# Kernel optimization log

Measured on AMD Instinct MI355X. Metric: run time of the kernel, lower is better.

Reference implementation:

```python
import jax, jax.numpy as jnp
from jax import lax
import numpy as np

T, N, E = 8, 20000, 640000
D_IN, H, K = 2, 64, 3


def setup_inputs() -> dict:
    key = jax.random.key(0)
    ks = jax.random.split(key, 10)
    x = jax.random.normal(ks[0], (T, N, D_IN), dtype=jnp.float32)
    edge_idx = jax.random.randint(ks[1], (T, 2, E), 0, N, dtype=jnp.int64)
    edge_attr = jax.random.uniform(ks[2], (T, E), dtype=jnp.float32)
    Fin = D_IN + H
    s = 0.05
    Wr = jax.random.normal(ks[3], (K, Fin, H), dtype=jnp.float32) * s
    Wu = jax.random.normal(ks[4], (K, Fin, H), dtype=jnp.float32) * s
    Wc = jax.random.normal(ks[5], (K, Fin, H), dtype=jnp.float32) * s
    br = jnp.zeros((H,), dtype=jnp.float32)
    bu = jnp.zeros((H,), dtype=jnp.float32)
    bc = jnp.zeros((H,), dtype=jnp.float32)
    return {"x": x, "edge_idx": edge_idx, "edge_attr": edge_attr,
            "Wr": Wr, "br": br, "Wu": Wu, "bu": bu, "Wc": Wc, "bc": bc}


def reference(x, edge_idx, edge_attr, Wr, br, Wu, bu, Wc, bc):
    n = x.shape[1]
    k_hops = Wr.shape[0]

    def cheb(v, src, dst, wn, W, b):
        # Chebyshev recursion on scaled Laplacian (PyG ChebConv, lambda_max=2)
        def prop(t):
            return jax.ops.segment_sum(wn[:, None] * t[src], dst, num_segments=n)
        Tx0 = v
        out = Tx0 @ W[0]
        Tx1 = prop(Tx0)
        out = out + Tx1 @ W[1]
        for kk in range(2, k_hops):
            Tx2 = 2.0 * prop(Tx1) - Tx0
            out = out + Tx2 @ W[kk]
            Tx0, Tx1 = Tx1, Tx2
        return out + b

    def step(h, inp):
        x_t, ei, w_t = inp
        src, dst = ei[0], ei[1]
        # sym-normalized Laplacian, scaled by 2/lambda_max=1; self-loop weight is 0
        deg = jax.ops.segment_sum(w_t, src, num_segments=n)
        safe = jnp.where(deg > 0, deg, 1.0)
        dinv = jnp.where(deg > 0, lax.rsqrt(safe), 0.0)
        wn = -dinv[src] * w_t * dinv[dst]
        comb = jnp.concatenate([x_t, h], axis=1)
        r = jax.nn.sigmoid(cheb(comb, src, dst, wn, Wr, br))
        u = jax.nn.sigmoid(cheb(comb, src, dst, wn, Wu, bu))
        c = jnp.tanh(cheb(jnp.concatenate([x_t, r * h], axis=1), src, dst, wn, Wc, bc))
        h_new = u * h + (1.0 - u) * c
        return h_new, None

    h0 = jnp.zeros((n, br.shape[0]), dtype=x.dtype)
    h_final, _ = lax.scan(step, h0, (x, edge_idx, edge_attr))
    return h_final
```

## Files before the change

### kernel.cpp

```cpp
#include <hip/hip_runtime.h>

#define NN 20000
#define EE 640000
#define TT 8
#define HF 64
#define AS 232
#define ACS 104
#define BSS 194
#define PBLK 5000
#define TILE 2560
#define NBIN 250
#define BWID 80
#define ECAP 3072
#define LCAP 24

typedef _Float16 f16;
typedef unsigned int uint;
typedef __attribute__((ext_vector_type(8))) _Float16 half8;
typedef __attribute__((ext_vector_type(4))) float floatx4;

__device__ __forceinline__ float lo16f(uint v) { return (float)__builtin_bit_cast(f16, (unsigned short)(v & 0xffff)); }
__device__ __forceinline__ float hi16f(uint v) { return (float)__builtin_bit_cast(f16, (unsigned short)(v >> 16)); }
__device__ __forceinline__ uint pk16(float a, float b) {
    unsigned short ua = __builtin_bit_cast(unsigned short, (f16)a);
    unsigned short ub = __builtin_bit_cast(unsigned short, (f16)b);
    return (uint)ua | ((uint)ub << 16);
}

__global__ __launch_bounds__(256) void k_prepW(
    const float* __restrict__ Wr, const float* __restrict__ Wu, const float* __restrict__ Wc,
    f16* __restrict__ Wp, f16* __restrict__ Wcp)
{
    int idx = blockIdx.x * 256 + threadIdx.x;
    if (idx < 8 * 7 * 64) {
        int lane = idx & 63;
        int kb = (idx >> 6) % 7;
        int nb = (idx >> 6) / 7;
        int col = nb * 16 + (lane & 15);
        int g = col >> 6, jj = col & 63;
        const float* W = (g == 0) ? Wr : Wu;
        half8 v;
        #pragma unroll
        for (int e = 0; e < 8; e++) {
            int k = kb * 32 + ((lane >> 4) << 3) + e;
            float val = 0.f;
            if (k < 192)      { int hop = k >> 6; int i = 2 + (k & 63); val = W[(hop * 66 + i) * 64 + jj]; }
            else if (k < 198) { int q = k - 192;  int hop = q >> 1;     val = W[(hop * 66 + (q & 1)) * 64 + jj]; }
            v[e] = (f16)val;
        }
        *(half8*)&Wp[(size_t)idx * 8] = v;
        return;
    }
    int idx2 = idx - 8 * 7 * 64;
    if (idx2 >= 12 * 3 * 64) return;
    int lane = idx2 & 63;
    int kb = (idx2 >> 6) % 3;
    int nbc = (idx2 >> 6) / 3;
    int col = nbc * 16 + (lane & 15);
    int mode = col >> 6, j = col & 63;
    half8 v;
    #pragma unroll
    for (int e = 0; e < 8; e++) {
        int k = kb * 32 + ((lane >> 4) << 3) + e;
        float val = 0.f;
        if (k < 66) {
            if (mode == 0)      val = Wc[(0 * 66 + k) * 64 + j] - Wc[(2 * 66 + k) * 64 + j];
            else if (mode == 1) val = Wc[(1 * 66 + k) * 64 + j];
            else                val = Wc[(2 * 66 + k) * 64 + j];
        }
        v[e] = (f16)val;
    }
    *(half8*)&Wcp[(size_t)idx2 * 8] = v;
}

__global__ __launch_bounds__(256) void k_setx(
    const float* __restrict__ x4, uint* __restrict__ xf4,
    int* __restrict__ binptr, int* __restrict__ sbinptr)
{
    int idx = blockIdx.x * 256 + threadIdx.x;
    if (idx < 4 * NBIN) { binptr[idx] = 0; sbinptr[idx] = 0; }
    if (idx >= 4 * NN) return;
    int tl = idx / NN, n = idx - tl * NN;
    xf4[idx] = pk16(x4[(size_t)tl * NN * 2 + 2 * n], x4[(size_t)tl * NN * 2 + 2 * n + 1]);
}

__global__ __launch_bounds__(256) void k_bin(
    const int* __restrict__ eidx, const float* __restrict__ eatt, int t0,
    int* __restrict__ binptr, uint2* __restrict__ ebuf,
    int* __restrict__ sbinptr, uint* __restrict__ sbuf)
{
    __shared__ uint2 buf[NBIN][LCAP];
    __shared__ uint  sbl[NBIN][LCAP];
    __shared__ int lcnt[NBIN], scnt[NBIN];
    __shared__ int scan[256];
    __shared__ int gb[NBIN];
    int tid = threadIdx.x;
    if (tid < NBIN) { lcnt[tid] = 0; scnt[tid] = 0; }
    __syncthreads();
    int tl = blockIdx.x / 250, tile = blockIdx.x % 250;
    const int*   src = eidx + (size_t)(t0 + tl) * 2 * EE + tile * TILE;
    const int*   dst = src + EE;
    const float* w   = eatt + (size_t)(t0 + tl) * EE + tile * TILE;
    int* bp = binptr + tl * NBIN;
    int* sp = sbinptr + tl * NBIN;
    size_t ebase = (size_t)tl * NBIN * ECAP;
    #pragma unroll
    for (int i = 0; i < TILE / 256; i++) {
        int e = i * 256 + tid;
        int s = __builtin_nontemporal_load(&src[e]);
        int d = __builtin_nontemporal_load(&dst[e]);
        float wv = __builtin_nontemporal_load(&w[e]);
        int bin = d / BWID;
        uint2 ent = make_uint2(((uint)d << 16) | (uint)s, __float_as_uint(wv));
        int p = atomicAdd(&lcnt[bin], 1);
        if (p < LCAP) buf[bin][p] = ent;
        else {
            int gp = atomicAdd(&bp[bin], 1);
            if (gp < ECAP) ebuf[ebase + (size_t)bin * ECAP + gp] = ent;
        }
        int sbin = s / BWID;
        uint sent = (pk16(wv, 0.f) << 16) | (uint)s;
        int sq = atomicAdd(&scnt[sbin], 1);
        if (sq < LCAP) sbl[sbin][sq] = sent;
        else {
            int gp = atomicAdd(&sp[sbin], 1);
            if (gp < ECAP) sbuf[ebase + (size_t)sbin * ECAP + gp] = sent;
        }
    }
    __syncthreads();
    {
        int c = (tid < NBIN) ? (lcnt[tid] < LCAP ? lcnt[tid] : LCAP) : 0;
        scan[tid] = c;
        __syncthreads();
        #pragma unroll
        for (int o = 1; o < 256; o <<= 1) {
            int v = (tid >= o) ? scan[tid - o] : 0;
            __syncthreads();
            scan[tid] += v;
            __syncthreads();
        }
        if (c > 0) gb[tid] = atomicAdd(&bp[tid], c);
        __syncthreads();
        int total = scan[255];
        for (int i = tid; i < total; i += 256) {
            int lo = 0, hi = 255;
            #pragma unroll
            for (int it = 0; it < 8; it++) { int mid = (lo + hi) >> 1; if (scan[mid] > i) hi = mid; else lo = mid + 1; }
            int p = i - (lo ? scan[lo - 1] : 0);
            int gp = gb[lo] + p;
            if (gp < ECAP) ebuf[ebase + (size_t)lo * ECAP + gp] = buf[lo][p];
        }
    }
    __syncthreads();
    {
        int c = (tid < NBIN) ? (scnt[tid] < LCAP ? scnt[tid] : LCAP) : 0;
        scan[tid] = c;
        __syncthreads();
        #pragma unroll
        for (int o = 1; o < 256; o <<= 1) {
            int v = (tid >= o) ? scan[tid - o] : 0;
            __syncthreads();
            scan[tid] += v;
            __syncthreads();
        }
        if (c > 0) gb[tid] = atomicAdd(&sp[tid], c);
        __syncthreads();
        int total = scan[255];
        for (int i = tid; i < total; i += 256) {
            int lo = 0, hi = 255;
            #pragma unroll
            for (int it = 0; it < 8; it++) { int mid = (lo + hi) >> 1; if (scan[mid] > i) hi = mid; else lo = mid + 1; }
            int p = i - (lo ? scan[lo - 1] : 0);
            int gp = gb[lo] + p;
            if (gp < ECAP) sbuf[ebase + (size_t)lo * ECAP + gp] = sbl[lo][p];
        }
    }
}

__global__ __launch_bounds__(256) void k_degred(
    const uint* __restrict__ sbuf, const int* __restrict__ sbinptr,
    float* __restrict__ dinv)
{
    __shared__ float dacc[BWID];
    int tl = blockIdx.x / NBIN, b = blockIdx.x % NBIN, tid = threadIdx.x;
    int nume = sbinptr[tl * NBIN + b]; if (nume > ECAP) nume = ECAP;
    if (tid < BWID) dacc[tid] = 0.f;
    __syncthreads();
    size_t base = (size_t)(tl * NBIN + b) * ECAP;
    for (int i = tid; i < nume; i += 256) {
        uint e = sbuf[base + i];
        atomicAdd(&dacc[(e & 0xffff) - b * BWID], hi16f(e));
    }
    __syncthreads();
    if (tid < BWID) {
        float d = dacc[tid];
        dinv[(size_t)tl * NN + b * BWID + tid] = d > 0.f ? 1.f / sqrtf(d) : 0.f;
    }
}

__global__ __launch_bounds__(256) void k_csr(
    const uint2* __restrict__ ebuf, const int* __restrict__ binptr,
    const float* __restrict__ dinv,
    uint* __restrict__ entries, int* __restrict__ row_ptr, int* __restrict__ cnt)
{
    __shared__ uint proc[ECAP];
    __shared__ unsigned char lnb[ECAP];
    __shared__ uint staged[ECAP];
    __shared__ int lcnt[BWID], loff[BWID];
    int tl = blockIdx.x / NBIN, b = blockIdx.x % NBIN, tid = threadIdx.x;
    int nume = binptr[tl * NBIN + b]; if (nume > ECAP) nume = ECAP;
    const float* dv = dinv + (size_t)tl * NN;
    size_t base = (size_t)(tl * NBIN + b) * ECAP;
    if (tid < BWID) lcnt[tid] = 0;
    __syncthreads();
    for (int i = tid; i < nume; i += 256) {
        uint2 ent = ebuf[base + i];
        int s = ent.x & 0xffff;
        int d = ent.x >> 16;
        float wv = __uint_as_float(ent.y);
        float wn = -dv[s] * wv * dv[d];
        unsigned short wb = __builtin_bit_cast(unsigned short, (f16)wn);
        proc[i] = ((uint)wb << 16) | (uint)s;
        int ln = d - b * BWID;
        lnb[i] = (unsigned char)ln;
        atomicAdd(&lcnt[ln], 1);
    }
    __syncthreads();
    if (tid == 0) {
        int run = 0;
        for (int i = 0; i < BWID; i++) { loff[i] = run; run += lcnt[i]; }
    }
    __syncthreads();
    if (tid < BWID) {
        int n = tl * NN + b * BWID + tid;
        row_ptr[n] = (int)base + loff[tid];
        cnt[n] = lcnt[tid];
    }
    __syncthreads();
    for (int i = tid; i < nume; i += 256) {
        int p = atomicAdd(&loff[lnb[i]], 1);
        staged[p] = proc[i];
    }
    __syncthreads();
    for (int i = tid; i < nume; i += 256)
        entries[base + i] = staged[i];
}

__device__ __forceinline__ void gather64(
    const f16* __restrict__ src_mat, const uint* wnb, int mp, int j, int q,
    float& s0, float& s1)
{
    float a0[8], a1[8];
    #pragma unroll
    for (int k = 0; k < 8; k++) { a0[k] = 0.f; a1[k] = 0.f; }
    for (int e = 0; e < mp; e += 32) {
        uint ee[16], rr[16];
        #pragma unroll
        for (int k = 0; k < 16; k++) ee[k] = wnb[e + 2 * k + q];
        #pragma unroll
        for (int k = 0; k < 16; k++) rr[k] = *(const uint*)&src_mat[(size_t)(ee[k] & 0xffff) * HF + 2 * j];
        #pragma unroll
        for (int k = 0; k < 16; k++) {
            float w = hi16f(ee[k]);
            a0[k & 7] += w * lo16f(rr[k]);
            a1[k & 7] += w * hi16f(rr[k]);
        }
    }
    s0 = ((a0[0] + a0[1]) + (a0[2] + a0[3])) + ((a0[4] + a0[5]) + (a0[6] + a0[7]));
    s1 = ((a1[0] + a1[1]) + (a1[2] + a1[3])) + ((a1[4] + a1[5]) + (a1[6] + a1[7]));
    s0 += __shfl_xor(s0, 32);
    s1 += __shfl_xor(s1, 32);
}

__global__ __launch_bounds__(256) void k_prop(
    const f16* __restrict__ src_mat, const f16* __restrict__ base,
    f16* __restrict__ dst,
    const int* __restrict__ row_ptr, const int* __restrict__ cnt,
    const uint* __restrict__ entries,
    float alpha, float beta,
    const uint* __restrict__ xsrc, const uint* __restrict__ xbase,
    uint* __restrict__ xdst)
{
    __shared__ uint wnbuf[4][128];
    int ws = threadIdx.x >> 6, lane = threadIdx.x & 63;
    int node = blockIdx.x * 4 + ws;
    int m = cnt[node]; if (m > 128) m = 128;
    int st = row_ptr[node];
    int mp = (m + 31) & ~31;
    for (int idx = lane; idx < mp; idx += 64)
        wnbuf[ws][idx] = (idx < m) ? entries[st + idx] : 0u;
    asm volatile("s_waitcnt lgkmcnt(0)" ::: "memory");

    int j = lane & 31, q = lane >> 5;
    float s0, s1;
    gather64(src_mat, wnbuf[ws], mp, j, q, s0, s1);
    if (q == 0) {
        float r0 = alpha * s0, r1 = alpha * s1;
        if (base) {
            uint bv = *(const uint*)&base[(size_t)node * HF + 2 * j];
            r0 += beta * lo16f(bv);
            r1 += beta * hi16f(bv);
        }
        *(uint*)&dst[(size_t)node * HF + 2 * j] = pk16(r0, r1);
    }

    if (xdst) {
        float xa0 = 0.f, xa1 = 0.f;
        for (int i = lane; i < mp; i += 64) {
            uint ent = wnbuf[ws][i];
            uint xv = xsrc[ent & 0xffff];
            float wn = hi16f(ent);
            xa0 += wn * lo16f(xv);
            xa1 += wn * hi16f(xv);
        }
        #pragma unroll
        for (int o = 32; o >= 1; o >>= 1) {
            xa0 += __shfl_xor(xa0, o);
            xa1 += __shfl_xor(xa1, o);
        }
        if (lane == 0) {
            float r0 = alpha * xa0, r1 = alpha * xa1;
            if (xbase) { uint bv = xbase[node]; r0 += beta * lo16f(bv); r1 += beta * hi16f(bv); }
            xdst[node] = pk16(r0, r1);
        }
    }
}

__global__ __launch_bounds__(256) void k_prop_fin(
    const f16* __restrict__ S, const f16* __restrict__ B0,
    const f16* __restrict__ u, const float* __restrict__ h_in,
    float* __restrict__ h_out, f16* __restrict__ hA_out,
    const int* __restrict__ row_ptr, const int* __restrict__ cnt,
    const uint* __restrict__ entries)
{
    __shared__ uint wnbuf[4][128];
    int ws = threadIdx.x >> 6, lane = threadIdx.x & 63;
    int node = blockIdx.x * 4 + ws;
    int m = cnt[node]; if (m > 128) m = 128;
    int st = row_ptr[node];
    int mp = (m + 31) & ~31;
    for (int idx = lane; idx < mp; idx += 64)
        wnbuf[ws][idx] = (idx < m) ? entries[st + idx] : 0u;
    asm volatile("s_waitcnt lgkmcnt(0)" ::: "memory");

    int j = lane & 31, q = lane >> 5;
    float s0, s1;
    gather64(S, wnbuf[ws], mp, j, q, s0, s1);
    if (q == 0) {
        uint b0v = *(const uint*)&B0[(size_t)node * HF + 2 * j];
        float c0 = tanhf(s0 + lo16f(b0v));
        float c1 = tanhf(s1 + hi16f(b0v));
        uint uv = *(const uint*)&u[(size_t)node * HF + 2 * j];
        float u0 = lo16f(uv), u1 = hi16f(uv);
        float2 hv = *(const float2*)&h_in[(size_t)node * HF + 2 * j];
        float hn0 = u0 * hv.x + (1.f - u0) * c0;
        float hn1 = u1 * hv.y + (1.f - u1) * c1;
        *(float2*)&h_out[(size_t)node * HF + 2 * j] = make_float2(hn0, hn1);
        *(uint*)&hA_out[(size_t)node * HF + 2 * j] = pk16(hn0, hn1);
    }
}

#define MFMA16(a, b, c) __builtin_amdgcn_mfma_f32_16x16x32_f16(a, b, c, 0, 0, 0)

__global__ __launch_bounds__(512) void k_ru(
    const f16* __restrict__ hA, const f16* __restrict__ t1, const f16* __restrict__ t2,
    const uint* __restrict__ xf, const uint* __restrict__ t1x, const uint* __restrict__ t2x,
    const f16* __restrict__ Wp, const f16* __restrict__ Wcp,
    const float* __restrict__ br, const float* __restrict__ bu, const float* __restrict__ bc,
    f16* __restrict__ u_out,
    f16* __restrict__ B0, f16* __restrict__ B1, f16* __restrict__ B2)
{
    __shared__ __attribute__((aligned(16))) f16 At[64][AS];
    __shared__ __attribute__((aligned(16))) f16 Ac[64][ACS];
    __shared__ f16 Ub[64][68];
    int n0 = blockIdx.x * 64;
    int tid = threadIdx.x;

    for (int idx = tid; idx < 64 * 8 * 3; idx += 512) {
        int a = idx >> 9, r = (idx >> 3) & 63, s = idx & 7;
        const f16* src = (a == 0) ? hA : (a == 1 ? t1 : t2);
        int gn = n0 + r;
        half8 v = {0, 0, 0, 0, 0, 0, 0, 0};
        if (gn < NN) v = *(const half8*)&src[(size_t)gn * HF + s * 8];
        *(half8*)&At[r][a * 64 + s * 8] = v;
    }
    for (int idx = tid; idx < 64 * 17; idx += 512) {
        int r = idx / 17, c = idx % 17;
        *(uint*)((char*)&At[r][198] + 4 * c) = 0u;
    }
    for (int idx = tid; idx < 64 * 3; idx += 512) {
        int r = idx & 63, a = idx >> 6;
        const uint* src = (a == 0) ? xf : (a == 1 ? t1x : t2x);
        int gn = n0 + r;
        uint v = 0;
        if (gn < NN) v = src[gn];
        *(uint*)&At[r][192 + 2 * a] = v;
    }
    for (int idx = tid; idx < 64; idx += 512) {
        int gn = n0 + idx;
        *(uint*)&Ac[idx][0] = (gn < NN) ? xf[gn] : 0u;
    }
    for (int idx = tid; idx < 64 * 15; idx += 512) {
        int r = idx / 15, c = idx % 15;
        *(uint*)((char*)&Ac[r][66] + 4 * c) = 0u;
    }
    __syncthreads();

    int wid = tid >> 6, lane = tid & 63;
    int mrow = (wid & 1) * 32;
    int nb0 = (wid >> 1) * 2;
    int arow = mrow + (lane & 15);
    int koff = (lane >> 4) << 3;
    floatx4 z = {0.f, 0.f, 0.f, 0.f};
    {
        floatx4 acc00 = z, acc01 = z, acc10 = z, acc11 = z;
        #pragma unroll
        for (int kb = 0; kb < 7; kb++) {
            half8 a0 = *(const half8*)&At[arow][kb * 32 + koff];
            half8 a1 = *(const half8*)&At[arow + 16][kb * 32 + koff];
            half8 b0 = *(const half8*)&Wp[(size_t)(((nb0    ) * 7 + kb) * 64 + lane) * 8];
            half8 b1 = *(const half8*)&Wp[(size_t)(((nb0 + 1) * 7 + kb) * 64 + lane) * 8];
            acc00 = MFMA16(a0, b0, acc00);
            acc10 = MFMA16(a1, b0, acc10);
            acc01 = MFMA16(a0, b1, acc01);
            acc11 = MFMA16(a1, b1, acc11);
        }
        bool isR = nb0 < 4;
        #pragma unroll
        for (int mi = 0; mi < 2; mi++) {
            #pragma unroll
            for (int ni = 0; ni < 2; ni++) {
                floatx4 a = (mi == 0) ? (ni == 0 ? acc00 : acc01) : (ni == 0 ? acc10 : acc11);
                int jj = ((nb0 + ni) * 16 + (lane & 15)) & 63;
                float bias = isR ? br[jj] : bu[jj];
                int rbase = mrow + mi * 16 + ((lane >> 4) << 2);
                #pragma unroll
                for (int e = 0; e < 4; e++) {
                    int rloc = rbase + e;
                    float s = 1.f / (1.f + __expf(-(a[e] + bias)));
                    if (isR) {
                        float hv = (float)At[rloc][jj];
                        Ac[rloc][2 + jj] = (f16)(s * hv);
                    } else {
                        Ub[rloc][jj] = (f16)s;
                    }
                }
            }
        }
    }
    __syncthreads();

    for (int idx = tid; idx < 64 * 32; idx += 512) {
        int n = idx >> 5, c = idx & 31;
        int gn = n0 + n;
        if (gn < NN) *(uint*)&u_out[(size_t)gn * HF + 2 * c] = *(uint*)&Ub[n][2 * c];
    }
    f16* Bs = &At[0][0];
    #pragma unroll
    for (int i = 0; i < 6; i++) {
        int t = wid * 6 + i;
        int nbc = t >> 2, mq = t & 3;
        int ar = mq * 16 + (lane & 15);
        floatx4 acc;
        float binit = (nbc < 4) ? bc[nbc * 16 + (lane & 15)] : 0.f;
        acc[0] = binit; acc[1] = binit; acc[2] = binit; acc[3] = binit;
        #pragma unroll
        for (int kb = 0; kb < 3; kb++) {
            half8 a = *(const half8*)&Ac[ar][kb * 32 + koff];
            half8 b = *(const half8*)&Wcp[(size_t)(((nbc * 3 + kb) * 64) + lane) * 8];
            acc = MFMA16(a, b, acc);
        }
        int rbase = mq * 16 + ((lane >> 4) << 2);
        int col = nbc * 16 + (lane & 15);
        #pragma unroll
        for (int e = 0; e < 4; e++)
            Bs[(size_t)(rbase + e) * BSS + col] = (f16)acc[e];
    }
    __syncthreads();

    for (int idx = tid; idx < 64 * 96; idx += 512) {
        int n = idx / 96, c = idx % 96;
        int gn = n0 + n;
        if (gn < NN) {
            int col = 2 * c;
            f16* Bdst = (col < 64) ? B0 : (col < 128 ? B1 : B2);
            *(uint*)&Bdst[(size_t)gn * HF + (col & 63)] = *(uint*)&Bs[(size_t)n * BSS + col];
        }
    }
}


extern "C" void kernel_launch(void* const* d_in, const int* in_sizes, int n_in,
                              void* d_out, int out_size, void* d_ws, size_t ws_size,
                              hipStream_t stream)
{
    const float* x    = (const float*)d_in[0];
    const int*   eidx = (const int*)d_in[1];
    const float* eatt = (const float*)d_in[2];
    const float* Wr   = (const float*)d_in[3];
    const float* br   = (const float*)d_in[4];
    const float* Wu   = (const float*)d_in[5];
    const float* bu   = (const float*)d_in[6];
    const float* Wc   = (const float*)d_in[7];
    const float* bc   = (const float*)d_in[8];

    char* ws = (char*)d_ws;
    size_t off = 0;
    auto alloc = [&](size_t bytes) -> void* {
        void* p = ws + off;
        off += (bytes + 255) & ~(size_t)255;
        return p;
    };
    const size_t FB = (size_t)NN * HF * 2;
    float* h_f32   = (float*)alloc((size_t)NN * HF * 4);
    f16*   hA      = (f16*)alloc(FB);
    f16*   t1      = (f16*)alloc(FB);
    f16*   t2      = (f16*)alloc(FB);
    f16*   u       = (f16*)alloc(FB);
    f16*   B0      = (f16*)alloc(FB);
    f16*   B1      = (f16*)alloc(FB);
    f16*   B2      = (f16*)alloc(FB);
    float* dinv    = (float*)alloc((size_t)4 * NN * 4);
    uint*  xf      = (uint*)alloc((size_t)TT * NN * 4);
    uint*  t1x     = (uint*)alloc((size_t)NN * 4);
    uint*  t2x     = (uint*)alloc((size_t)NN * 4);
    int*   binptr  = (int*)alloc((size_t)4 * NBIN * 4);
    int*   sbinptr = (int*)alloc((size_t)4 * NBIN * 4);
    uint2* ebuf    = (uint2*)alloc((size_t)4 * NBIN * ECAP * 8);
    uint*  sbuf    = (uint*)alloc((size_t)4 * NBIN * ECAP * 4);
    uint*  entr    = (uint*)alloc((size_t)4 * NBIN * ECAP * 4);
    int*   rowp    = (int*)alloc((size_t)4 * NN * 4);
    int*   cnt     = (int*)alloc((size_t)4 * NN * 4);
    f16*   Wp      = (f16*)alloc((size_t)8 * 7 * 64 * 8 * 2);
    f16*   Wcp     = (f16*)alloc((size_t)12 * 3 * 64 * 8 * 2);

    hipMemsetAsync(h_f32, 0, (size_t)NN * HF * 4 + FB, stream);
    k_prepW<<<30, 256, 0, stream>>>(Wr, Wu, Wc, Wp, Wcp);

    const int GB = (NN + 63) / 64;
    const int DB = (4 * NN + 255) / 256;

    for (int half = 0; half < 2; ++half) {
        int t0 = half * 4;
        k_setx  <<<DB, 256, 0, stream>>>(x + (size_t)t0 * NN * 2, xf + (size_t)t0 * NN,
                                         binptr, sbinptr);
        k_bin   <<<1000, 256, 0, stream>>>(eidx, eatt, t0, binptr, ebuf, sbinptr, sbuf);
        k_degred<<<1000, 256, 0, stream>>>(sbuf, sbinptr, dinv);
        k_csr   <<<1000, 256, 0, stream>>>(ebuf, binptr, dinv, entr, rowp, cnt);

        for (int tl = 0; tl < 4; ++tl) {
            int t = t0 + tl;
            const int* rp = rowp + (size_t)tl * NN;
            const int* cp = cnt + (size_t)tl * NN;
            uint* xft = xf + (size_t)t * NN;

            k_prop<<<PBLK, 256, 0, stream>>>(hA, nullptr, t1, rp, cp, entr, 1.f,  0.f, xft, nullptr, t1x);
            k_prop<<<PBLK, 256, 0, stream>>>(t1, hA,      t2, rp, cp, entr, 2.f, -1.f, t1x, xft,     t2x);

            k_ru<<<GB, 512, 0, stream>>>(hA, t1, t2, xft, t1x, t2x, Wp, Wcp,
                                         br, bu, bc, u, B0, B1, B2);

            k_prop<<<PBLK, 256, 0, stream>>>(B2, B1, t2, rp, cp, entr, 2.f, 1.f, nullptr, nullptr, nullptr);

            float* hdst = (t == TT - 1) ? (float*)d_out : h_f32;
            k_prop_fin<<<PBLK, 256, 0, stream>>>(t2, B0, u, h_f32, hdst, hA, rp, cp, entr);
        }
    }
}
```

Measured before the change: 744.9 us.

## Replace global bin atomics with per-tile slot arrays and spill buffer

The edge binning kernel now writes each block's local per-bin buffers straight into fixed per-tile slots with per-tile counts, instead of scanning and using global atomics to compact into per-bin buffers. Overflow edges go to one small spill list per timestep, which the degree and CSR kernels scan and filter. The consumer kernels gather from 250 tile slots per bin and do a prefix scan to place entries. Timesteps are batched in groups of two instead of four, and x packing becomes a single upfront kernel. This trades contended global atomics and scan work in k_bin for more scattered reads in the consumers and a spill list that every block must scan.

```diff
diff --git a/kernel.cpp b/kernel.cpp
--- a/kernel.cpp
+++ b/kernel.cpp
@@ -13,9 +13,13 @@
 #define BWID 80
 #define ECAP 3072
 #define LCAP 24
+#define TB 2
+#define SPCAP 4096
 
 typedef _Float16 f16;
 typedef unsigned int uint;
+typedef unsigned char uchar;
+typedef unsigned long long ull;
 typedef __attribute__((ext_vector_type(8))) _Float16 half8;
 typedef __attribute__((ext_vector_type(4))) float floatx4;
 
@@ -73,27 +77,23 @@
     *(half8*)&Wcp[(size_t)idx2 * 8] = v;
 }
 
-__global__ __launch_bounds__(256) void k_setx(
-    const float* __restrict__ x4, uint* __restrict__ xf4,
-    int* __restrict__ binptr, int* __restrict__ sbinptr)
+__global__ __launch_bounds__(256) void k_pack(
+    const float* __restrict__ x, uint* __restrict__ xf)
 {
     int idx = blockIdx.x * 256 + threadIdx.x;
-    if (idx < 4 * NBIN) { binptr[idx] = 0; sbinptr[idx] = 0; }
-    if (idx >= 4 * NN) return;
-    int tl = idx / NN, n = idx - tl * NN;
-    xf4[idx] = pk16(x4[(size_t)tl * NN * 2 + 2 * n], x4[(size_t)tl * NN * 2 + 2 * n + 1]);
+    if (idx < TT * NN) xf[idx] = pk16(x[2 * idx], x[2 * idx + 1]);
 }
 
 __global__ __launch_bounds__(256) void k_bin(
     const int* __restrict__ eidx, const float* __restrict__ eatt, int t0,
-    int* __restrict__ binptr, uint2* __restrict__ ebuf,
-    int* __restrict__ sbinptr, uint* __restrict__ sbuf)
+    ull* __restrict__ dslot, uchar* __restrict__ dcnt_,
+    uint* __restrict__ sslot, uchar* __restrict__ scnt_,
+    ull* __restrict__ dsp, int* __restrict__ spn,
+    uint* __restrict__ ssp, int* __restrict__ ssn)
 {
     __shared__ uint2 buf[NBIN][LCAP];
     __shared__ uint  sbl[NBIN][LCAP];
     __shared__ int lcnt[NBIN], scnt[NBIN];
-    __shared__ int scan[256];
-    __shared__ int gb[NBIN];
     int tid = threadIdx.x;
     if (tid < NBIN) { lcnt[tid] = 0; scnt[tid] = 0; }
     __syncthreads();
@@ -101,9 +101,6 @@
     const int*   src = eidx + (size_t)(t0 + tl) * 2 * EE + tile * TILE;
     const int*   dst = src + EE;
     const float* w   = eatt + (size_t)(t0 + tl) * EE + tile * TILE;
-    int* bp = binptr + tl * NBIN;
-    int* sp = sbinptr + tl * NBIN;
-    size_t ebase = (size_t)tl * NBIN * ECAP;
     #pragma unroll
     for (int i = 0; i < TILE / 256; i++) {
         int e = i * 256 + tid;
@@ -111,85 +108,60 @@
         int d = __builtin_nontemporal_load(&dst[e]);
         float wv = __builtin_nontemporal_load(&w[e]);
         int bin = d / BWID;
-        uint2 ent = make_uint2(((uint)d << 16) | (uint)s, __float_as_uint(wv));
         int p = atomicAdd(&lcnt[bin], 1);
-        if (p < LCAP) buf[bin][p] = ent;
+        if (p < LCAP) buf[bin][p] = make_uint2(((uint)d << 16) | (uint)s, __float_as_uint(wv));
         else {
-            int gp = atomicAdd(&bp[bin], 1);
-            if (gp < ECAP) ebuf[ebase + (size_t)bin * ECAP + gp] = ent;
+            int gp = atomicAdd(&spn[tl], 1);
+            if (gp < SPCAP) dsp[(size_t)tl * SPCAP + gp] =
+                (ull)__float_as_uint(wv) << 32 | (((uint)d << 16) | (uint)s);
         }
         int sbin = s / BWID;
         uint sent = (pk16(wv, 0.f) << 16) | (uint)s;
         int sq = atomicAdd(&scnt[sbin], 1);
         if (sq < LCAP) sbl[sbin][sq] = sent;
         else {
-            int gp = atomicAdd(&sp[sbin], 1);
-            if (gp < ECAP) sbuf[ebase + (size_t)sbin * ECAP + gp] = sent;
-        }
-    }
-    __syncthreads();
-    {
-        int c = (tid < NBIN) ? (lcnt[tid] < LCAP ? lcnt[tid] : LCAP) : 0;
-        scan[tid] = c;
-        __syncthreads();
-        #pragma unroll
-        for (int o = 1; o < 256; o <<= 1) {
-            int v = (tid >= o) ? scan[tid - o] : 0;
-            __syncthreads();
-            scan[tid] += v;
-            __syncthreads();
-        }
-        if (c > 0) gb[tid] = atomicAdd(&bp[tid], c);
-        __syncthreads();
-        int total = scan[255];
-        for (int i = tid; i < total; i += 256) {
-            int lo = 0, hi = 255;
-            #pragma unroll
-            for (int it = 0; it < 8; it++) { int mid = (lo + hi) >> 1; if (scan[mid] > i) hi = mid; else lo = mid + 1; }
-            int p = i - (lo ? scan[lo - 1] : 0);
-            int gp = gb[lo] + p;
-            if (gp < ECAP) ebuf[ebase + (size_t)lo * ECAP + gp] = buf[lo][p];
-        }
-    }
-    __syncthreads();
-    {
-        int c = (tid < NBIN) ? (scnt[tid] < LCAP ? scnt[tid] : LCAP) : 0;
-        scan[tid] = c;
-        __syncthreads();
-        #pragma unroll
-        for (int o = 1; o < 256; o <<= 1) {
-            int v = (tid >= o) ? scan[tid - o] : 0;
-            __syncthreads();
-            scan[tid] += v;
-            __syncthreads();
-        }
-        if (c > 0) gb[tid] = atomicAdd(&sp[tid], c);
-        __syncthreads();
-        int total = scan[255];
-        for (int i = tid; i < total; i += 256) {
-            int lo = 0, hi = 255;
-            #pragma unroll
-            for (int it = 0; it < 8; it++) { int mid = (lo + hi) >> 1; if (scan[mid] > i) hi = mid; else lo = mid + 1; }
-            int p = i - (lo ? scan[lo - 1] : 0);
-            int gp = gb[lo] + p;
-            if (gp < ECAP) sbuf[ebase + (size_t)lo * ECAP + gp] = sbl[lo][p];
-        }
+            int gp = atomicAdd(&ssn[tl], 1);
+            if (gp < SPCAP) ssp[(size_t)tl * SPCAP + gp] = sent;
+        }
+    }
+    __syncthreads();
+    size_t base = (size_t)blockIdx.x * (NBIN * LCAP);
+    const ull* bufl = (const ull*)&buf[0][0];
+    for (int idx = tid; idx < NBIN * LCAP; idx += 256)
+        __builtin_nontemporal_store(bufl[idx], &dslot[base + idx]);
+    const uint* sbll = &sbl[0][0];
+    for (int idx = tid; idx < NBIN * LCAP; idx += 256)
+        __builtin_nontemporal_store(sbll[idx], &sslot[base + idx]);
+    if (tid < NBIN) {
+        dcnt_[blockIdx.x * 256 + tid] = (uchar)(lcnt[tid] < LCAP ? lcnt[tid] : LCAP);
+        scnt_[blockIdx.x * 256 + tid] = (uchar)(scnt[tid] < LCAP ? scnt[tid] : LCAP);
     }
 }
 
 __global__ __launch_bounds__(256) void k_degred(
-    const uint* __restrict__ sbuf, const int* __restrict__ sbinptr,
+    const uint* __restrict__ sslot, const uchar* __restrict__ scnt_,
+    const uint* __restrict__ ssp, const int* __restrict__ ssn,
     float* __restrict__ dinv)
 {
     __shared__ float dacc[BWID];
+    __shared__ uchar cs[256];
     int tl = blockIdx.x / NBIN, b = blockIdx.x % NBIN, tid = threadIdx.x;
-    int nume = sbinptr[tl * NBIN + b]; if (nume > ECAP) nume = ECAP;
     if (tid < BWID) dacc[tid] = 0.f;
-    __syncthreads();
-    size_t base = (size_t)(tl * NBIN + b) * ECAP;
-    for (int i = tid; i < nume; i += 256) {
-        uint e = sbuf[base + i];
-        atomicAdd(&dacc[(e & 0xffff) - b * BWID], hi16f(e));
+    if (tid < 256) cs[tid] = (tid < 250) ? scnt_[(tl * 250 + tid) * 256 + b] : 0;
+    __syncthreads();
+    for (int idx = tid; idx < 250 * LCAP; idx += 256) {
+        int t = idx / LCAP, p = idx % LCAP;
+        if (p < (int)cs[t]) {
+            uint e = __builtin_nontemporal_load(
+                &sslot[((size_t)(tl * 250 + t) * NBIN + b) * LCAP + p]);
+            atomicAdd(&dacc[(e & 0xffff) - b * BWID], hi16f(e));
+        }
+    }
+    int nsp = ssn[tl]; if (nsp > SPCAP) nsp = SPCAP;
+    for (int i = tid; i < nsp; i += 256) {
+        uint e = ssp[(size_t)tl * SPCAP + i];
+        int s = e & 0xffff;
+        if (s / BWID == b) atomicAdd(&dacc[s - b * BWID], hi16f(e));
     }
     __syncthreads();
     if (tid < BWID) {
@@ -199,38 +171,77 @@
 }
 
 __global__ __launch_bounds__(256) void k_csr(
-    const uint2* __restrict__ ebuf, const int* __restrict__ binptr,
+    const ull* __restrict__ dslot, const uchar* __restrict__ dcnt_,
+    const ull* __restrict__ dsp, const int* __restrict__ spn,
     const float* __restrict__ dinv,
     uint* __restrict__ entries, int* __restrict__ row_ptr, int* __restrict__ cnt)
 {
     __shared__ uint proc[ECAP];
-    __shared__ unsigned char lnb[ECAP];
+    __shared__ uchar lnb[ECAP];
     __shared__ uint staged[ECAP];
     __shared__ int lcnt[BWID], loff[BWID];
+    __shared__ uchar cs[256];
+    __shared__ int sscan[256];
+    __shared__ int extr;
     int tl = blockIdx.x / NBIN, b = blockIdx.x % NBIN, tid = threadIdx.x;
-    int nume = binptr[tl * NBIN + b]; if (nume > ECAP) nume = ECAP;
     const float* dv = dinv + (size_t)tl * NN;
-    size_t base = (size_t)(tl * NBIN + b) * ECAP;
     if (tid < BWID) lcnt[tid] = 0;
-    __syncthreads();
-    for (int i = tid; i < nume; i += 256) {
-        uint2 ent = ebuf[base + i];
-        int s = ent.x & 0xffff;
-        int d = ent.x >> 16;
-        float wv = __uint_as_float(ent.y);
-        float wn = -dv[s] * wv * dv[d];
-        unsigned short wb = __builtin_bit_cast(unsigned short, (f16)wn);
-        proc[i] = ((uint)wb << 16) | (uint)s;
-        int ln = d - b * BWID;
-        lnb[i] = (unsigned char)ln;
-        atomicAdd(&lcnt[ln], 1);
-    }
-    __syncthreads();
+    cs[tid] = (tid < 250) ? dcnt_[(tl * 250 + tid) * 256 + b] : 0;
+    __syncthreads();
+    int c = (int)cs[tid];
+    sscan[tid] = c;
+    __syncthreads();
+    #pragma unroll
+    for (int o = 1; o < 256; o <<= 1) {
+        int v = (tid >= o) ? sscan[tid - o] : 0;
+        __syncthreads();
+        sscan[tid] += v;
+        __syncthreads();
+    }
+    if (tid == 0) extr = sscan[255];
+    for (int idx = tid; idx < 250 * LCAP; idx += 256) {
+        int t = idx / LCAP, p = idx % LCAP;
+        if (p < (int)cs[t]) {
+            int pos = sscan[t] - (int)cs[t] + p;
+            if (pos < ECAP) {
+                ull ev = __builtin_nontemporal_load(
+                    &dslot[((size_t)(tl * 250 + t) * NBIN + b) * LCAP + p]);
+                int s = (uint)ev & 0xffff, d = ((uint)ev) >> 16;
+                float wn = -dv[s] * __uint_as_float((uint)(ev >> 32)) * dv[d];
+                unsigned short wb = __builtin_bit_cast(unsigned short, (f16)wn);
+                proc[pos] = ((uint)wb << 16) | (uint)s;
+                int ln = d - b * BWID;
+                lnb[pos] = (uchar)ln;
+                atomicAdd(&lcnt[ln], 1);
+            }
+        }
+    }
+    __syncthreads();
+    int nsp = spn[tl]; if (nsp > SPCAP) nsp = SPCAP;
+    for (int i = tid; i < nsp; i += 256) {
+        ull ev = dsp[(size_t)tl * SPCAP + i];
+        int d = ((uint)ev) >> 16;
+        if (d / BWID == b) {
+            int pos = atomicAdd(&extr, 1);
+            if (pos < ECAP) {
+                int s = (uint)ev & 0xffff;
+                float wn = -dv[s] * __uint_as_float((uint)(ev >> 32)) * dv[d];
+                unsigned short wb = __builtin_bit_cast(unsigned short, (f16)wn);
+                proc[pos] = ((uint)wb << 16) | (uint)s;
+                int ln = d - b * BWID;
+                lnb[pos] = (uchar)ln;
+                atomicAdd(&lcnt[ln], 1);
+            }
+        }
+    }
+    __syncthreads();
+    int nume = extr; if (nume > ECAP) nume = ECAP;
     if (tid == 0) {
         int run = 0;
         for (int i = 0; i < BWID; i++) { loff[i] = run; run += lcnt[i]; }
     }
     __syncthreads();
+    size_t base = (size_t)(tl * NBIN + b) * ECAP;
     if (tid < BWID) {
         int n = tl * NN + b * BWID + tid;
         row_ptr[n] = (int)base + loff[tid];
@@ -512,43 +523,47 @@
         return p;
     };
     const size_t FB = (size_t)NN * HF * 2;
-    float* h_f32   = (float*)alloc((size_t)NN * HF * 4);
-    f16*   hA      = (f16*)alloc(FB);
-    f16*   t1      = (f16*)alloc(FB);
-    f16*   t2      = (f16*)alloc(FB);
-    f16*   u       = (f16*)alloc(FB);
-    f16*   B0      = (f16*)alloc(FB);
-    f16*   B1      = (f16*)alloc(FB);
-    f16*   B2      = (f16*)alloc(FB);
-    float* dinv    = (float*)alloc((size_t)4 * NN * 4);
-    uint*  xf      = (uint*)alloc((size_t)TT * NN * 4);
-    uint*  t1x     = (uint*)alloc((size_t)NN * 4);
-    uint*  t2x     = (uint*)alloc((size_t)NN * 4);
-    int*   binptr  = (int*)alloc((size_t)4 * NBIN * 4);
-    int*   sbinptr = (int*)alloc((size_t)4 * NBIN * 4);
-    uint2* ebuf    = (uint2*)alloc((size_t)4 * NBIN * ECAP * 8);
-    uint*  sbuf    = (uint*)alloc((size_t)4 * NBIN * ECAP * 4);
-    uint*  entr    = (uint*)alloc((size_t)4 * NBIN * ECAP * 4);
-    int*   rowp    = (int*)alloc((size_t)4 * NN * 4);
-    int*   cnt     = (int*)alloc((size_t)4 * NN * 4);
-    f16*   Wp      = (f16*)alloc((size_t)8 * 7 * 64 * 8 * 2);
-    f16*   Wcp     = (f16*)alloc((size_t)12 * 3 * 64 * 8 * 2);
+    float* h_f32  = (float*)alloc((size_t)NN * HF * 4);
+    f16*   hA     = (f16*)alloc(FB);
+    f16*   t1     = (f16*)alloc(FB);
+    f16*   t2     = (f16*)alloc(FB);
+    f16*   u      = (f16*)alloc(FB);
+    f16*   B0     = (f16*)alloc(FB);
+    f16*   B1     = (f16*)alloc(FB);
+    f16*   B2     = (f16*)alloc(FB);
+    float* dinv   = (float*)alloc((size_t)TB * NN * 4);
+    uint*  xf     = (uint*)alloc((size_t)TT * NN * 4);
+    uint*  t1x    = (uint*)alloc((size_t)NN * 4);
+    uint*  t2x    = (uint*)alloc((size_t)NN * 4);
+    ull*   dslot  = (ull*)alloc((size_t)TB * 250 * NBIN * LCAP * 8);
+    uint*  sslot  = (uint*)alloc((size_t)TB * 250 * NBIN * LCAP * 4);
+    uchar* dcnt_  = (uchar*)alloc((size_t)TB * 250 * 256);
+    uchar* scnt_  = (uchar*)alloc((size_t)TB * 250 * 256);
+    ull*   dsp    = (ull*)alloc((size_t)TB * SPCAP * 8);
+    uint*  ssp    = (uint*)alloc((size_t)TB * SPCAP * 4);
+    int*   spz    = (int*)alloc(256);
+    uint*  entr   = (uint*)alloc((size_t)TB * NBIN * ECAP * 4);
+    int*   rowp   = (int*)alloc((size_t)TB * NN * 4);
+    int*   cnt    = (int*)alloc((size_t)TB * NN * 4);
+    f16*   Wp     = (f16*)alloc((size_t)8 * 7 * 64 * 8 * 2);
+    f16*   Wcp    = (f16*)alloc((size_t)12 * 3 * 64 * 8 * 2);
+    int*   spn = spz, *ssn = spz + 2;
 
     hipMemsetAsync(h_f32, 0, (size_t)NN * HF * 4 + FB, stream);
     k_prepW<<<30, 256, 0, stream>>>(Wr, Wu, Wc, Wp, Wcp);
+    k_pack <<<(TT * NN + 255) / 256, 256, 0, stream>>>(x, xf);
 
     const int GB = (NN + 63) / 64;
-    const int DB = (4 * NN + 255) / 256;
-
-    for (int half = 0; half < 2; ++half) {
-        int t0 = half * 4;
-        k_setx  <<<DB, 256, 0, stream>>>(x + (size_t)t0 * NN * 2, xf + (size_t)t0 * NN,
-                                         binptr, sbinptr);
-        k_bin   <<<1000, 256, 0, stream>>>(eidx, eatt, t0, binptr, ebuf, sbinptr, sbuf);
-        k_degred<<<1000, 256, 0, stream>>>(sbuf, sbinptr, dinv);
-        k_csr   <<<1000, 256, 0, stream>>>(ebuf, binptr, dinv, entr, rowp, cnt);
-
-        for (int tl = 0; tl < 4; ++tl) {
+
+    for (int qtr = 0; qtr < 4; ++qtr) {
+        int t0 = qtr * TB;
+        hipMemsetAsync(spz, 0, 16, stream);
+        k_bin   <<<TB * 250, 256, 0, stream>>>(eidx, eatt, t0, dslot, dcnt_, sslot, scnt_,
+                                               dsp, spn, ssp, ssn);
+        k_degred<<<TB * NBIN, 256, 0, stream>>>(sslot, scnt_, ssp, ssn, dinv);
+        k_csr   <<<TB * NBIN, 256, 0, stream>>>(dslot, dcnt_, dsp, spn, dinv, entr, rowp, cnt);
+
+        for (int tl = 0; tl < TB; ++tl) {
             int t = t0 + tl;
             const int* rp = rowp + (size_t)tl * NN;
             const int* cp = cnt + (size_t)tl * NN;
```

New measurement: 820.2 us. 1.1x slower.

## Build all timestep graphs in one pass and shrink gather padding granularity

Applied to the files above, without the earlier changes.

The edge binning, degree reduction and CSR construction now run once over all 8 timesteps instead of twice over groups of 4. This fills the GPU with twice as many blocks and removes the per-half setup launches, at the cost of doubling the workspace for edge buffers. The propagation gather now pads neighbor lists to multiples of 8 instead of 32. It uses a 16-wide main loop plus an 8-wide tail, so fewer zero-weight padded rows are fetched, at the cost of smaller unroll depth per iteration.

```diff
diff --git a/kernel.cpp b/kernel.cpp
--- a/kernel.cpp
+++ b/kernel.cpp
@@ -16,6 +16,7 @@
 
 typedef _Float16 f16;
 typedef unsigned int uint;
+typedef unsigned char uchar;
 typedef __attribute__((ext_vector_type(8))) _Float16 half8;
 typedef __attribute__((ext_vector_type(4))) float floatx4;
 
@@ -73,19 +74,15 @@
     *(half8*)&Wcp[(size_t)idx2 * 8] = v;
 }
 
-__global__ __launch_bounds__(256) void k_setx(
-    const float* __restrict__ x4, uint* __restrict__ xf4,
-    int* __restrict__ binptr, int* __restrict__ sbinptr)
+__global__ __launch_bounds__(256) void k_pack(
+    const float* __restrict__ x, uint* __restrict__ xf)
 {
     int idx = blockIdx.x * 256 + threadIdx.x;
-    if (idx < 4 * NBIN) { binptr[idx] = 0; sbinptr[idx] = 0; }
-    if (idx >= 4 * NN) return;
-    int tl = idx / NN, n = idx - tl * NN;
-    xf4[idx] = pk16(x4[(size_t)tl * NN * 2 + 2 * n], x4[(size_t)tl * NN * 2 + 2 * n + 1]);
+    if (idx < TT * NN) xf[idx] = pk16(x[2 * idx], x[2 * idx + 1]);
 }
 
 __global__ __launch_bounds__(256) void k_bin(
-    const int* __restrict__ eidx, const float* __restrict__ eatt, int t0,
+    const int* __restrict__ eidx, const float* __restrict__ eatt,
     int* __restrict__ binptr, uint2* __restrict__ ebuf,
     int* __restrict__ sbinptr, uint* __restrict__ sbuf)
 {
@@ -98,9 +95,9 @@
     if (tid < NBIN) { lcnt[tid] = 0; scnt[tid] = 0; }
     __syncthreads();
     int tl = blockIdx.x / 250, tile = blockIdx.x % 250;
-    const int*   src = eidx + (size_t)(t0 + tl) * 2 * EE + tile * TILE;
+    const int*   src = eidx + (size_t)tl * 2 * EE + tile * TILE;
     const int*   dst = src + EE;
-    const float* w   = eatt + (size_t)(t0 + tl) * EE + tile * TILE;
+    const float* w   = eatt + (size_t)tl * EE + tile * TILE;
     int* bp = binptr + tl * NBIN;
     int* sp = sbinptr + tl * NBIN;
     size_t ebase = (size_t)tl * NBIN * ECAP;
@@ -204,7 +201,7 @@
     uint* __restrict__ entries, int* __restrict__ row_ptr, int* __restrict__ cnt)
 {
     __shared__ uint proc[ECAP];
-    __shared__ unsigned char lnb[ECAP];
+    __shared__ uchar lnb[ECAP];
     __shared__ uint staged[ECAP];
     __shared__ int lcnt[BWID], loff[BWID];
     int tl = blockIdx.x / NBIN, b = blockIdx.x % NBIN, tid = threadIdx.x;
@@ -222,7 +219,7 @@
         unsigned short wb = __builtin_bit_cast(unsigned short, (f16)wn);
         proc[i] = ((uint)wb << 16) | (uint)s;
         int ln = d - b * BWID;
-        lnb[i] = (unsigned char)ln;
+        lnb[i] = (uchar)ln;
         atomicAdd(&lcnt[ln], 1);
     }
     __syncthreads();
@@ -253,17 +250,31 @@
     float a0[8], a1[8];
     #pragma unroll
     for (int k = 0; k < 8; k++) { a0[k] = 0.f; a1[k] = 0.f; }
-    for (int e = 0; e < mp; e += 32) {
-        uint ee[16], rr[16];
-        #pragma unroll
-        for (int k = 0; k < 16; k++) ee[k] = wnb[e + 2 * k + q];
-        #pragma unroll
-        for (int k = 0; k < 16; k++) rr[k] = *(const uint*)&src_mat[(size_t)(ee[k] & 0xffff) * HF + 2 * j];
-        #pragma unroll
-        for (int k = 0; k < 16; k++) {
+    int e = 0;
+    for (; e + 16 <= mp; e += 16) {
+        uint ee[8], rr[8];
+        #pragma unroll
+        for (int k = 0; k < 8; k++) ee[k] = wnb[e + 2 * k + q];
+        #pragma unroll
+        for (int k = 0; k < 8; k++) rr[k] = *(const uint*)&src_mat[(size_t)(ee[k] & 0xffff) * HF + 2 * j];
+        #pragma unroll
+        for (int k = 0; k < 8; k++) {
             float w = hi16f(ee[k]);
-            a0[k & 7] += w * lo16f(rr[k]);
-            a1[k & 7] += w * hi16f(rr[k]);
+            a0[k] += w * lo16f(rr[k]);
+            a1[k] += w * hi16f(rr[k]);
+        }
+    }
+    for (; e < mp; e += 8) {
+        uint ee[4], rr[4];
+        #pragma unroll
+        for (int k = 0; k < 4; k++) ee[k] = wnb[e + 2 * k + q];
+        #pragma unroll
+        for (int k = 0; k < 4; k++) rr[k] = *(const uint*)&src_mat[(size_t)(ee[k] & 0xffff) * HF + 2 * j];
+        #pragma unroll
+        for (int k = 0; k < 4; k++) {
+            float w = hi16f(ee[k]);
+            a0[k] += w * lo16f(rr[k]);
+            a1[k] += w * hi16f(rr[k]);
         }
     }
     s0 = ((a0[0] + a0[1]) + (a0[2] + a0[3])) + ((a0[4] + a0[5]) + (a0[6] + a0[7]));
@@ -286,7 +297,7 @@
     int node = blockIdx.x * 4 + ws;
     int m = cnt[node]; if (m > 128) m = 128;
     int st = row_ptr[node];
-    int mp = (m + 31) & ~31;
+    int mp = (m + 7) & ~7;
     for (int idx = lane; idx < mp; idx += 64)
         wnbuf[ws][idx] = (idx < m) ? entries[st + idx] : 0u;
     asm volatile("s_waitcnt lgkmcnt(0)" ::: "memory");
@@ -338,7 +349,7 @@
     int node = blockIdx.x * 4 + ws;
     int m = cnt[node]; if (m > 128) m = 128;
     int st = row_ptr[node];
-    int mp = (m + 31) & ~31;
+    int mp = (m + 7) & ~7;
     for (int idx = lane; idx < mp; idx += 64)
         wnbuf[ws][idx] = (idx < m) ? entries[st + idx] : 0u;
     asm volatile("s_waitcnt lgkmcnt(0)" ::: "memory");
@@ -520,50 +531,46 @@
     f16*   B0      = (f16*)alloc(FB);
     f16*   B1      = (f16*)alloc(FB);
     f16*   B2      = (f16*)alloc(FB);
-    float* dinv    = (float*)alloc((size_t)4 * NN * 4);
+    float* dinv    = (float*)alloc((size_t)TT * NN * 4);
     uint*  xf      = (uint*)alloc((size_t)TT * NN * 4);
     uint*  t1x     = (uint*)alloc((size_t)NN * 4);
     uint*  t2x     = (uint*)alloc((size_t)NN * 4);
-    int*   binptr  = (int*)alloc((size_t)4 * NBIN * 4);
-    int*   sbinptr = (int*)alloc((size_t)4 * NBIN * 4);
-    uint2* ebuf    = (uint2*)alloc((size_t)4 * NBIN * ECAP * 8);
-    uint*  sbuf    = (uint*)alloc((size_t)4 * NBIN * ECAP * 4);
-    uint*  entr    = (uint*)alloc((size_t)4 * NBIN * ECAP * 4);
-    int*   rowp    = (int*)alloc((size_t)4 * NN * 4);
-    int*   cnt     = (int*)alloc((size_t)4 * NN * 4);
+    int*   bptr2   = (int*)alloc((size_t)2 * TT * NBIN * 4);
+    uint2* ebuf    = (uint2*)alloc((size_t)TT * NBIN * ECAP * 8);
+    uint*  sbuf    = (uint*)alloc((size_t)TT * NBIN * ECAP * 4);
+    uint*  entr    = (uint*)alloc((size_t)TT * NBIN * ECAP * 4);
+    int*   rowp    = (int*)alloc((size_t)TT * NN * 4);
+    int*   cnt     = (int*)alloc((size_t)TT * NN * 4);
     f16*   Wp      = (f16*)alloc((size_t)8 * 7 * 64 * 8 * 2);
     f16*   Wcp     = (f16*)alloc((size_t)12 * 3 * 64 * 8 * 2);
+    int* binptr = bptr2;
+    int* sbinptr = bptr2 + TT * NBIN;
 
     hipMemsetAsync(h_f32, 0, (size_t)NN * HF * 4 + FB, stream);
+    hipMemsetAsync(bptr2, 0, (size_t)2 * TT * NBIN * 4, stream);
     k_prepW<<<30, 256, 0, stream>>>(Wr, Wu, Wc, Wp, Wcp);
+    k_pack <<<(TT * NN + 255) / 256, 256, 0, stream>>>(x, xf);
+
+    k_bin   <<<TT * 250, 256, 0, stream>>>(eidx, eatt, binptr, ebuf, sbinptr, sbuf);
+    k_degred<<<TT * NBIN, 256, 0, stream>>>(sbuf, sbinptr, dinv);
+    k_csr   <<<TT * NBIN, 256, 0, stream>>>(ebuf, binptr, dinv, entr, rowp, cnt);
 
     const int GB = (NN + 63) / 64;
-    const int DB = (4 * NN + 255) / 256;
-
-    for (int half = 0; half < 2; ++half) {
-        int t0 = half * 4;
-        k_setx  <<<DB, 256, 0, stream>>>(x + (size_t)t0 * NN * 2, xf + (size_t)t0 * NN,
-                                         binptr, sbinptr);
-        k_bin   <<<1000, 256, 0, stream>>>(eidx, eatt, t0, binptr, ebuf, sbinptr, sbuf);
-        k_degred<<<1000, 256, 0, stream>>>(sbuf, sbinptr, dinv);
-        k_csr   <<<1000, 256, 0, stream>>>(ebuf, binptr, dinv, entr, rowp, cnt);
-
-        for (int tl = 0; tl < 4; ++tl) {
-            int t = t0 + tl;
-            const int* rp = rowp + (size_t)tl * NN;
-            const int* cp = cnt + (size_t)tl * NN;
-            uint* xft = xf + (size_t)t * NN;
-
-            k_prop<<<PBLK, 256, 0, stream>>>(hA, nullptr, t1, rp, cp, entr, 1.f,  0.f, xft, nullptr, t1x);
-            k_prop<<<PBLK, 256, 0, stream>>>(t1, hA,      t2, rp, cp, entr, 2.f, -1.f, t1x, xft,     t2x);
-
-            k_ru<<<GB, 512, 0, stream>>>(hA, t1, t2, xft, t1x, t2x, Wp, Wcp,
-                                         br, bu, bc, u, B0, B1, B2);
-
-            k_prop<<<PBLK, 256, 0, stream>>>(B2, B1, t2, rp, cp, entr, 2.f, 1.f, nullptr, nullptr, nullptr);
-
-            float* hdst = (t == TT - 1) ? (float*)d_out : h_f32;
-            k_prop_fin<<<PBLK, 256, 0, stream>>>(t2, B0, u, h_f32, hdst, hA, rp, cp, entr);
-        }
-    }
-}
+
+    for (int t = 0; t < TT; ++t) {
+        const int* rp = rowp + (size_t)t * NN;
+        const int* cp = cnt + (size_t)t * NN;
+        uint* xft = xf + (size_t)t * NN;
+
+        k_prop<<<PBLK, 256, 0, stream>>>(hA, nullptr, t1, rp, cp, entr, 1.f,  0.f, xft, nullptr, t1x);
+        k_prop<<<PBLK, 256, 0, stream>>>(t1, hA,      t2, rp, cp, entr, 2.f, -1.f, t1x, xft,     t2x);
+
+        k_ru<<<GB, 512, 0, stream>>>(hA, t1, t2, xft, t1x, t2x, Wp, Wcp,
+                                     br, bu, bc, u, B0, B1, B2);
+
+        k_prop<<<PBLK, 256, 0, stream>>>(B2, B1, t2, rp, cp, entr, 2.f, 1.f, nullptr, nullptr, nullptr);
+
+        float* hdst = (t == TT - 1) ? (float*)d_out : h_f32;
+        k_prop_fin<<<PBLK, 256, 0, stream>>>(t2, B0, u, h_f32, hdst, hA, rp, cp, entr);
+    }
+}
```

After: 699.8 us. 1.06x faster.
